# Kernel tuning notes

Hardware: AMD Instinct MI355X
Metric: run time of the kernel (lower is better)

Reference implementation:

```python
import jax, jax.numpy as jnp
import numpy as np

N_HEADS, D_MODEL, D_K, D_V = 16, 1024, 64, 64
B, S = 2, 2048

def setup_inputs() -> dict:
    key = jax.random.key(0)
    k = jax.random.split(key, 7)
    s = 1.0 / np.sqrt(D_MODEL)
    return {
        "input_Q": jax.random.normal(k[0], (B, S, D_MODEL), jnp.float32),
        "input_K": jax.random.normal(k[1], (B, S, D_MODEL), jnp.float32),
        "input_V": jax.random.normal(k[2], (B, S, D_MODEL), jnp.float32),
        "W_Q": jax.random.normal(k[3], (D_MODEL, N_HEADS * D_K), jnp.float32) * s,
        "W_K": jax.random.normal(k[4], (D_MODEL, N_HEADS * D_K), jnp.float32) * s,
        "W_V": jax.random.normal(k[5], (D_MODEL, N_HEADS * D_V), jnp.float32) * s,
        "W_O": jax.random.normal(k[6], (N_HEADS * D_V, D_MODEL), jnp.float32) * s,
    }

def reference(input_Q, input_K, input_V, W_Q, W_K, W_V, W_O):
    b = input_Q.shape[0]
    # project and split heads: [b, h, s, d]
    Q = (input_Q @ W_Q).reshape(b, -1, N_HEADS, D_K).transpose(0, 2, 1, 3)
    K = (input_K @ W_K).reshape(b, -1, N_HEADS, D_K).transpose(0, 2, 1, 3)
    V = (input_V @ W_V).reshape(b, -1, N_HEADS, D_V).transpose(0, 2, 1, 3)
    scores = jnp.einsum("bhqd,bhkd->bhqk", Q, K) / np.sqrt(D_K)
    attn = jax.nn.softmax(scores, axis=-1)
    context = jnp.einsum("bhqk,bhkd->bhqd", attn, V)
    context = context.transpose(0, 2, 1, 3).reshape(b, -1, N_HEADS * D_V)
    out = context @ W_O + input_Q  # residual
    # LayerNorm instantiated fresh in torch forward -> gamma=1, beta=0
    mu = jnp.mean(out, axis=-1, keepdims=True)
    var = jnp.var(out, axis=-1, keepdims=True)
    return (out - mu) / jnp.sqrt(var + 1e-5)
```

## Files before the change

kernel.cpp:

```cpp
#include <hip/hip_runtime.h>
#include <hip/hip_bf16.h>
#include <cstdint>
#include <cstddef>

#define DEVFN __device__ __forceinline__

typedef __attribute__((ext_vector_type(8))) short short8;
typedef __attribute__((ext_vector_type(4))) float f32x4;
typedef __attribute__((ext_vector_type(16))) float f32x16;
typedef __attribute__((ext_vector_type(4))) unsigned short us4;

static constexpr int S_LEN = 2048;
static constexpr int DM    = 1024;
static constexpr int H     = 16;
static constexpr int DK    = 64;
static constexpr int BATCH = 2;
static constexpr int MROWS = BATCH * S_LEN;

DEVFN unsigned short f2bf(float f) {
  union { float f; unsigned int u; } x; x.f = f;
  unsigned int r = x.u + 0x7fffu + ((x.u >> 16) & 1u);
  return (unsigned short)(r >> 16);
}

DEVFN float fast_exp2(float x) { return __builtin_amdgcn_exp2f(x); }

DEVFN f32x4 mfma16(short8 a, short8 b, f32x4 c) {
  return __builtin_amdgcn_mfma_f32_16x16x32_bf16(a, b, c, 0, 0, 0);
}

DEVFN f32x16 mfma32(short8 a, short8 b, f32x16 c) {
  return __builtin_amdgcn_mfma_f32_32x32x16_bf16(a, b, c, 0, 0, 0);
}

DEVFN unsigned int cvtpk(float lo, float hi) {
  unsigned int r;
  asm("v_cvt_pk_bf16_f32 %0, %1, %2" : "=v"(r) : "v"(lo), "v"(hi));
  return r;
}

DEVFN void gload_lds16(const void* g, void* l) {
  __builtin_amdgcn_global_load_lds(
      (const __attribute__((address_space(1))) void*)g,
      (__attribute__((address_space(3))) void*)l, 16, 0, 0);
}

__global__ __launch_bounds__(256) void wt_transpose(
    const float* __restrict__ Wq, const float* __restrict__ Wk,
    const float* __restrict__ Wv, const float* __restrict__ Wo,
    unsigned short* __restrict__ Tq, unsigned short* __restrict__ Tk,
    unsigned short* __restrict__ Tv, unsigned short* __restrict__ To)
{
  const float* W = blockIdx.z == 0 ? Wq : blockIdx.z == 1 ? Wk : blockIdx.z == 2 ? Wv : Wo;
  unsigned short* T = blockIdx.z == 0 ? Tq : blockIdx.z == 1 ? Tk : blockIdx.z == 2 ? Tv : To;
  __shared__ float tile[32][33];
  int n0 = blockIdx.x * 32, k0 = blockIdx.y * 32;
  int tx = threadIdx.x & 31, ty = threadIdx.x >> 5;
#pragma unroll
  for (int i = 0; i < 4; ++i)
    tile[ty + 8 * i][tx] = W[(size_t)(k0 + ty + 8 * i) * DM + n0 + tx];
  __syncthreads();
#pragma unroll
  for (int i = 0; i < 4; ++i) {
    int n = ty + 8 * i;
    T[(size_t)(n0 + n) * DM + k0 + tx] = f2bf(tile[tx][n]);
  }
}

__global__ __launch_bounds__(256) void xcvt3(
    const float* __restrict__ X0, const float* __restrict__ X1,
    const float* __restrict__ X2, unsigned short* __restrict__ Y)
{
  const float* X = blockIdx.y == 0 ? X0 : blockIdx.y == 1 ? X1 : X2;
  unsigned short* Yz = Y + (size_t)blockIdx.y * MROWS * DM;
  const size_t i = ((size_t)blockIdx.x * 256 + threadIdx.x) * 8;
  float4 v0 = *(const float4*)(X + i);
  float4 v1 = *(const float4*)(X + i + 4);
  union { us4 u[2]; short8 s; } r;
  r.u[0].x = f2bf(v0.x); r.u[0].y = f2bf(v0.y); r.u[0].z = f2bf(v0.z); r.u[0].w = f2bf(v0.w);
  r.u[1].x = f2bf(v1.x); r.u[1].y = f2bf(v1.y); r.u[1].z = f2bf(v1.z); r.u[1].w = f2bf(v1.w);
  *(short8*)(Yz + i) = r.s;
}

__global__ __launch_bounds__(256, 3) void gemm_qkv(
    const unsigned short* __restrict__ Xb,
    const unsigned short* __restrict__ Tq, const unsigned short* __restrict__ Tk,
    const unsigned short* __restrict__ Tv,
    unsigned short* __restrict__ Qb, unsigned short* __restrict__ Kb,
    unsigned short* __restrict__ Vt)
{
  __shared__ __align__(16) unsigned short As[2][128 * 32];
  __shared__ __align__(16) unsigned short Bs[2][128 * 32];

  const int z = blockIdx.z;
  const unsigned short* A = Xb + (size_t)z * MROWS * DM;
  const unsigned short* T = z == 0 ? Tq : z == 1 ? Tk : Tv;

  const int tid = threadIdx.x;
  const int lane = tid & 63, w = tid >> 6;
  const int wm = w >> 1, wn = w & 1;
  const int lr = lane & 15, lg = lane >> 4;
  const int m0 = blockIdx.x * 128, n0 = blockIdx.y * 128;

  const int srw = lane >> 2, sch = lane & 3;

  auto stage = [&](int buf, int k0) {
#pragma unroll
    for (int i = 0; i < 2; ++i) {
      const int rr = (w * 2 + i) * 16 + srw;
      const int sc = (sch ^ ((rr >> 1) & 3)) * 8;
      gload_lds16(A + (size_t)(m0 + rr) * DM + k0 + sc, &As[buf][(w * 2 + i) * 512]);
      gload_lds16(T + (size_t)(n0 + rr) * DM + k0 + sc, &Bs[buf][(w * 2 + i) * 512]);
    }
  };

  f32x4 acc[4][4];
#pragma unroll
  for (int m = 0; m < 4; ++m)
#pragma unroll
    for (int n = 0; n < 4; ++n) acc[m][n] = (f32x4){0.f, 0.f, 0.f, 0.f};

  stage(0, 0);
  __syncthreads();

  int buf = 0;
  for (int kt = 0; kt < DM / 32; ++kt) {
    if (kt + 1 < DM / 32) stage(buf ^ 1, (kt + 1) * 32);
    short8 af[4], bfr[4];
#pragma unroll
    for (int m = 0; m < 4; ++m) {
      const int row = wm * 64 + m * 16 + lr;
      const int ch = lg ^ ((row >> 1) & 3);
      af[m] = *(const short8*)&As[buf][row * 32 + ch * 8];
    }
#pragma unroll
    for (int n = 0; n < 4; ++n) {
      const int row = wn * 64 + n * 16 + lr;
      const int ch = lg ^ ((row >> 1) & 3);
      bfr[n] = *(const short8*)&Bs[buf][row * 32 + ch * 8];
    }
#pragma unroll
    for (int m = 0; m < 4; ++m)
#pragma unroll
      for (int n = 0; n < 4; ++n) acc[m][n] = mfma16(af[m], bfr[n], acc[m][n]);
    __syncthreads();
    buf ^= 1;
  }

  if (z < 2) {
    const float scale = (z == 0) ? 0.125f * 1.44269504088896f : 1.0f;
    unsigned short* out = z == 0 ? Qb : Kb;
#pragma unroll
    for (int m = 0; m < 4; ++m)
#pragma unroll
      for (int n = 0; n < 4; ++n) {
        int col = n0 + wn * 64 + n * 16 + lr;
        int h = col >> 6, d = col & 63;
#pragma unroll
        for (int r = 0; r < 4; ++r) {
          int row = m0 + wm * 64 + m * 16 + lg * 4 + r;
          int b = row >> 11, s = row & (S_LEN - 1);
          out[((size_t)(b * H + h) * S_LEN + s) * DK + d] = f2bf(acc[m][n][r] * scale);
        }
      }
  } else {
#pragma unroll
    for (int m = 0; m < 4; ++m)
#pragma unroll
      for (int n = 0; n < 4; ++n) {
        int col = n0 + wn * 64 + n * 16 + lr;
        int h = col >> 6, d = col & 63;
        int row = m0 + wm * 64 + m * 16 + lg * 4;
        int b = row >> 11, s = row & (S_LEN - 1);
        us4 u;
#pragma unroll
        for (int r = 0; r < 4; ++r) u[r] = f2bf(acc[m][n][r]);
        *(us4*)(Vt + ((size_t)(b * H + h) * DK + d) * S_LEN + s) = u;
      }
  }
}

__global__ __launch_bounds__(256, 2) void attn(
    const unsigned short* __restrict__ Qg, const unsigned short* __restrict__ Kg,
    const unsigned short* __restrict__ Vg, unsigned short* __restrict__ ctx)
{
  constexpr int KBLK = 64;
  constexpr int NT = S_LEN / KBLK;
  __shared__ __align__(16) unsigned short Ks[2][KBLK][DK];
  __shared__ __align__(16) unsigned short Vs[2][DK][KBLK];

  const int tid = threadIdx.x, lane = tid & 63, w = tid >> 6;
  const int l31 = lane & 31, hi = lane >> 5;

  const int orig = blockIdx.x;
  const int id = (orig & 7) * 64 + (orig >> 3);
  const int bh = id >> 4, qb = id & 15;
  const int b = bh >> 4, h = bh & 15;
  const int q = qb * 128 + w * 32 + l31;

  const unsigned short* Qbh = Qg + (size_t)bh * S_LEN * DK;
  const unsigned short* Kbh = Kg + (size_t)bh * S_LEN * DK;
  const unsigned short* Vbh = Vg + (size_t)bh * DK * S_LEN;

  const int srow = lane >> 3;
  const int sslot = ((lane & 7) ^ srow) * 8;

  auto stage = [&](int buf, int t) {
    const int kbase = t * KBLK;
#pragma unroll
    for (int c = 0; c < 2; ++c) {
      const int rbase = w * 8 + c * 32;
      gload_lds16(Kbh + (size_t)(kbase + rbase + srow) * DK + sslot, &Ks[buf][rbase][0]);
      gload_lds16(Vbh + (size_t)(rbase + srow) * S_LEN + kbase + sslot, &Vs[buf][rbase][0]);
    }
  };

  short8 qf[4];
#pragma unroll
  for (int kk = 0; kk < 4; ++kk)
    qf[kk] = *(const short8*)(Qbh + (size_t)q * DK + kk * 16 + hi * 8);

  f32x16 o0, o1;
#pragma unroll
  for (int i = 0; i < 16; ++i) { o0[i] = 0.f; o1[i] = 0.f; }
  float lrun = 0.f;

  const int swz = (l31 & 7) << 4;

  stage(0, 0);
  __syncthreads();

  int buf = 0;
  for (int t = 0; t < NT; ++t) {
    if (t + 1 < NT) stage(buf ^ 1, t + 1);

    const char* Kb = (const char*)&Ks[buf][0][0];
    const char* Vb = (const char*)&Vs[buf][0][0];

    f32x16 s0, s1;
#pragma unroll
    for (int i = 0; i < 16; ++i) { s0[i] = 0.f; s1[i] = 0.f; }
#pragma unroll
    for (int kk = 0; kk < 4; ++kk) {
      const int cb = (kk * 32 + hi * 16) ^ swz;
      short8 ka0 = *(const short8*)(Kb + l31 * 128 + cb);
      short8 ka1 = *(const short8*)(Kb + (32 + l31) * 128 + cb);
      s0 = mfma32(ka0, qf[kk], s0);
      s1 = mfma32(ka1, qf[kk], s1);
    }

#pragma unroll
    for (int i = 0; i < 16; ++i) {
      s0[i] = fast_exp2(s0[i]);
      s1[i] = fast_exp2(s1[i]);
    }

    float d0[16];
#pragma unroll
    for (int i = 0; i < 16; ++i) d0[i] = s0[i] + s1[i];
#pragma unroll
    for (int st = 8; st >= 1; st >>= 1)
#pragma unroll
      for (int i = 0; i < st; ++i) d0[i] = d0[i] + d0[i + st];
    lrun += d0[0] + __shfl_xor(d0[0], 32, 64);

    short8 pf[4];
#pragma unroll
    for (int sl = 0; sl < 4; ++sl) {
      const f32x16& sv = (sl & 2) ? s1 : s0;
      const int base = (sl & 1) * 8;
      const unsigned int a01 = cvtpk(sv[base + 0], sv[base + 1]);
      const unsigned int a23 = cvtpk(sv[base + 2], sv[base + 3]);
      const unsigned int b01 = cvtpk(sv[base + 4], sv[base + 5]);
      const unsigned int b23 = cvtpk(sv[base + 6], sv[base + 7]);
      const unsigned int x0 = __shfl_xor(hi ? a01 : b01, 32, 64);
      const unsigned int x1 = __shfl_xor(hi ? a23 : b23, 32, 64);
      union { unsigned int u[4]; short8 v; } pu;
      pu.u[0] = hi ? x0 : a01;
      pu.u[1] = hi ? x1 : a23;
      pu.u[2] = hi ? b01 : x0;
      pu.u[3] = hi ? b23 : x1;
      pf[sl] = pu.v;
    }

#pragma unroll
    for (int sl = 0; sl < 4; ++sl) {
      const int cb = (sl * 32 + hi * 16) ^ swz;
      short8 va0 = *(const short8*)(Vb + l31 * 128 + cb);
      short8 va1 = *(const short8*)(Vb + (32 + l31) * 128 + cb);
      o0 = mfma32(va0, pf[sl], o0);
      o1 = mfma32(va1, pf[sl], o1);
    }

    __syncthreads();
    buf ^= 1;
  }

  const float rinv = 1.0f / lrun;
  unsigned short* crow = ctx + ((size_t)(b * S_LEN + q)) * DM + h * DK;
#pragma unroll
  for (int n = 0; n < 2; ++n) {
#pragma unroll
    for (int r = 0; r < 16; r += 2) {
      const float v0 = (n ? o1[r] : o0[r]) * rinv;
      const float v1 = (n ? o1[r + 1] : o0[r + 1]) * rinv;
      const int d = (r & 3) + 8 * (r >> 2) + 4 * hi + 32 * n;
      *(unsigned int*)(crow + d) = cvtpk(v0, v1);
    }
  }
}

__global__ __launch_bounds__(256, 3) void gemm_out(
    const unsigned short* __restrict__ C, const unsigned short* __restrict__ To,
    const float* __restrict__ resid, float* __restrict__ y)
{
  __shared__ __align__(16) unsigned short As[2][128 * 32];
  __shared__ __align__(16) unsigned short Bs[2][64 * 32];

  const int tid = threadIdx.x;
  const int lane = tid & 63, w = tid >> 6;
  const int wm = w >> 1, wn = w & 1;
  const int lr = lane & 15, lg = lane >> 4;
  const int m0 = blockIdx.x * 128, n0 = blockIdx.y * 64;

  const int brr = lane >> 2, bsc = lane & 3;

  auto stage = [&](int buf, int k0) {
#pragma unroll
    for (int i = 0; i < 2; ++i) {
      const int rr = (w * 2 + i) * 16 + brr;
      const int sc = (bsc ^ ((rr >> 1) & 3)) * 8;
      gload_lds16(C + (size_t)(m0 + rr) * DM + k0 + sc, &As[buf][(w * 2 + i) * 512]);
    }
    const int rr = w * 16 + brr;
    const int sc = (bsc ^ ((rr >> 1) & 3)) * 8;
    gload_lds16(To + (size_t)(n0 + rr) * DM + k0 + sc, &Bs[buf][w * 512]);
  };

  f32x4 acc[4][2];
#pragma unroll
  for (int m = 0; m < 4; ++m)
#pragma unroll
    for (int n = 0; n < 2; ++n) acc[m][n] = (f32x4){0.f, 0.f, 0.f, 0.f};

  stage(0, 0);
  __syncthreads();

  int buf = 0;
  for (int kt = 0; kt < DM / 32; ++kt) {
    if (kt + 1 < DM / 32) stage(buf ^ 1, (kt + 1) * 32);
    short8 af[4], bfr[2];
#pragma unroll
    for (int m = 0; m < 4; ++m) {
      const int row = wm * 64 + m * 16 + lr;
      const int ch = lg ^ ((row >> 1) & 3);
      af[m] = *(const short8*)&As[buf][row * 32 + ch * 8];
    }
#pragma unroll
    for (int n = 0; n < 2; ++n) {
      const int row = wn * 32 + n * 16 + lr;
      const int ch = lg ^ ((row >> 1) & 3);
      bfr[n] = *(const short8*)&Bs[buf][row * 32 + ch * 8];
    }
#pragma unroll
    for (int m = 0; m < 4; ++m)
#pragma unroll
      for (int n = 0; n < 2; ++n) acc[m][n] = mfma16(af[m], bfr[n], acc[m][n]);
    __syncthreads();
    buf ^= 1;
  }

#pragma unroll
  for (int m = 0; m < 4; ++m)
#pragma unroll
    for (int n = 0; n < 2; ++n) {
      int col = n0 + wn * 32 + n * 16 + lr;
#pragma unroll
      for (int r = 0; r < 4; ++r) {
        int row = m0 + wm * 64 + m * 16 + lg * 4 + r;
        size_t idx = (size_t)row * DM + col;
        y[idx] = acc[m][n][r] + resid[idx];
      }
    }
}

__global__ __launch_bounds__(256) void lnorm(const float* __restrict__ y, float* __restrict__ out)
{
  const int row = blockIdx.x;
  const int tid = threadIdx.x;
  const float4 v = ((const float4*)(y + (size_t)row * DM))[tid];
  float s = v.x + v.y + v.z + v.w;
  float sq = v.x * v.x + v.y * v.y + v.z * v.z + v.w * v.w;
  s += __shfl_xor(s, 1, 64);  sq += __shfl_xor(sq, 1, 64);
  s += __shfl_xor(s, 2, 64);  sq += __shfl_xor(sq, 2, 64);
  s += __shfl_xor(s, 4, 64);  sq += __shfl_xor(sq, 4, 64);
  s += __shfl_xor(s, 8, 64);  sq += __shfl_xor(sq, 8, 64);
  s += __shfl_xor(s, 16, 64); sq += __shfl_xor(sq, 16, 64);
  s += __shfl_xor(s, 32, 64); sq += __shfl_xor(sq, 32, 64);
  __shared__ float ps[4], pq[4];
  int w = tid >> 6, lane = tid & 63;
  if (lane == 0) { ps[w] = s; pq[w] = sq; }
  __syncthreads();
  s = ps[0] + ps[1] + ps[2] + ps[3];
  sq = pq[0] + pq[1] + pq[2] + pq[3];
  float mean = s * (1.0f / DM);
  float var = sq * (1.0f / DM) - mean * mean;
  float rstd = rsqrtf(var + 1e-5f);
  float4 ov;
  ov.x = (v.x - mean) * rstd;
  ov.y = (v.y - mean) * rstd;
  ov.z = (v.z - mean) * rstd;
  ov.w = (v.w - mean) * rstd;
  ((float4*)(out + (size_t)row * DM))[tid] = ov;
}

extern "C" void kernel_launch(void* const* d_in, const int* in_sizes, int n_in,
                              void* d_out, int out_size, void* d_ws, size_t ws_size,
                              hipStream_t stream) {
  const float* Xq = (const float*)d_in[0];
  const float* Xk = (const float*)d_in[1];
  const float* Xv = (const float*)d_in[2];
  const float* Wq = (const float*)d_in[3];
  const float* Wk = (const float*)d_in[4];
  const float* Wv = (const float*)d_in[5];
  const float* Wo = (const float*)d_in[6];
  float* out = (float*)d_out;
  char* ws = (char*)d_ws;

  const size_t WT_BYTES  = (size_t)DM * DM * 2;
  const size_t XB_BYTES  = (size_t)3 * MROWS * DM * 2;
  const size_t QKV_BYTES = (size_t)BATCH * H * S_LEN * DK * 2;

  size_t off = 0;
  auto take = [&](size_t bytes) { size_t o = off; off += (bytes + 255) & ~(size_t)255; return o; };
  unsigned short* Tq  = (unsigned short*)(ws + take(WT_BYTES));
  unsigned short* Tk  = (unsigned short*)(ws + take(WT_BYTES));
  unsigned short* Tv  = (unsigned short*)(ws + take(WT_BYTES));
  unsigned short* To  = (unsigned short*)(ws + take(WT_BYTES));
  size_t xb_off = take(XB_BYTES);
  unsigned short* Xb  = (unsigned short*)(ws + xb_off);
  unsigned short* Qb  = (unsigned short*)(ws + take(QKV_BYTES));
  unsigned short* Kb  = (unsigned short*)(ws + take(QKV_BYTES));
  unsigned short* Vt  = (unsigned short*)(ws + take(QKV_BYTES));
  unsigned short* Ctx = Xb;
  float* y = (float*)(ws + xb_off + (size_t)MROWS * DM * 2);

  if (ws_size < off) return;

  wt_transpose<<<dim3(32, 32, 4), 256, 0, stream>>>(Wq, Wk, Wv, Wo, Tq, Tk, Tv, To);
  xcvt3<<<dim3(2048, 3), 256, 0, stream>>>(Xq, Xk, Xv, Xb);
  gemm_qkv<<<dim3(32, 8, 3), 256, 0, stream>>>(Xb, Tq, Tk, Tv, Qb, Kb, Vt);
  attn<<<dim3(512), 256, 0, stream>>>(Qb, Kb, Vt, Ctx);
  gemm_out<<<dim3(32, 16), 256, 0, stream>>>(Ctx, To, Xq, y);
  lnorm<<<MROWS, 256, 0, stream>>>(y, out);
}
```

Before: 136.9 us.

## Load K and V fragments directly from global memory in attention loop

Removes the double-buffered LDS staging of K and V tiles, along with the async global-to-LDS copies and per-iteration barriers. Each wave now reads its MFMA operand fragments straight from global memory, relying on the caches. This eliminates synchronization and LDS traffic, but every wave fetches the same tiles independently and software prefetch overlap is lost.

```diff
diff --git a/kernel.cpp b/kernel.cpp
--- a/kernel.cpp
+++ b/kernel.cpp
@@ -186,8 +186,6 @@
 {
   constexpr int KBLK = 64;
   constexpr int NT = S_LEN / KBLK;
-  __shared__ __align__(16) unsigned short Ks[2][KBLK][DK];
-  __shared__ __align__(16) unsigned short Vs[2][DK][KBLK];
 
   const int tid = threadIdx.x, lane = tid & 63, w = tid >> 6;
   const int l31 = lane & 31, hi = lane >> 5;
@@ -199,21 +197,10 @@
   const int q = qb * 128 + w * 32 + l31;
 
   const unsigned short* Qbh = Qg + (size_t)bh * S_LEN * DK;
-  const unsigned short* Kbh = Kg + (size_t)bh * S_LEN * DK;
-  const unsigned short* Vbh = Vg + (size_t)bh * DK * S_LEN;
-
-  const int srow = lane >> 3;
-  const int sslot = ((lane & 7) ^ srow) * 8;
-
-  auto stage = [&](int buf, int t) {
-    const int kbase = t * KBLK;
-#pragma unroll
-    for (int c = 0; c < 2; ++c) {
-      const int rbase = w * 8 + c * 32;
-      gload_lds16(Kbh + (size_t)(kbase + rbase + srow) * DK + sslot, &Ks[buf][rbase][0]);
-      gload_lds16(Vbh + (size_t)(rbase + srow) * S_LEN + kbase + sslot, &Vs[buf][rbase][0]);
-    }
-  };
+  const unsigned short* K0 = Kg + (size_t)bh * S_LEN * DK + (size_t)l31 * DK + hi * 8;
+  const unsigned short* K1 = K0 + 32 * DK;
+  const unsigned short* V0 = Vg + (size_t)bh * DK * S_LEN + (size_t)l31 * S_LEN + hi * 8;
+  const unsigned short* V1 = V0 + 32 * S_LEN;
 
   short8 qf[4];
 #pragma unroll
@@ -225,26 +212,16 @@
   for (int i = 0; i < 16; ++i) { o0[i] = 0.f; o1[i] = 0.f; }
   float lrun = 0.f;
 
-  const int swz = (l31 & 7) << 4;
-
-  stage(0, 0);
-  __syncthreads();
-
-  int buf = 0;
   for (int t = 0; t < NT; ++t) {
-    if (t + 1 < NT) stage(buf ^ 1, t + 1);
-
-    const char* Kb = (const char*)&Ks[buf][0][0];
-    const char* Vb = (const char*)&Vs[buf][0][0];
+    const int kbase = t * KBLK;
 
     f32x16 s0, s1;
 #pragma unroll
     for (int i = 0; i < 16; ++i) { s0[i] = 0.f; s1[i] = 0.f; }
 #pragma unroll
     for (int kk = 0; kk < 4; ++kk) {
-      const int cb = (kk * 32 + hi * 16) ^ swz;
-      short8 ka0 = *(const short8*)(Kb + l31 * 128 + cb);
-      short8 ka1 = *(const short8*)(Kb + (32 + l31) * 128 + cb);
+      short8 ka0 = *(const short8*)(K0 + (size_t)kbase * DK + kk * 16);
+      short8 ka1 = *(const short8*)(K1 + (size_t)kbase * DK + kk * 16);
       s0 = mfma32(ka0, qf[kk], s0);
       s1 = mfma32(ka1, qf[kk], s1);
     }
@@ -285,15 +262,11 @@
 
 #pragma unroll
     for (int sl = 0; sl < 4; ++sl) {
-      const int cb = (sl * 32 + hi * 16) ^ swz;
-      short8 va0 = *(const short8*)(Vb + l31 * 128 + cb);
-      short8 va1 = *(const short8*)(Vb + (32 + l31) * 128 + cb);
+      short8 va0 = *(const short8*)(V0 + kbase + sl * 16);
+      short8 va1 = *(const short8*)(V1 + kbase + sl * 16);
       o0 = mfma32(va0, pf[sl], o0);
       o1 = mfma32(va1, pf[sl], o1);
     }
-
-    __syncthreads();
-    buf ^= 1;
   }
 
   const float rinv = 1.0f / lrun;
```

Result: slower. 202.1 us (+47.6%).
